# Kernel tuning notes

Hardware: AMD Instinct MI355X
Metric: run time of the kernel (lower is better)

Reference implementation:

```python
import jax, jax.numpy as jnp
import numpy as np

OUTPUT_DIM = 2000
INPUT_DIM = 8192
N_COLS = 2000  # must equal OUTPUT_DIM so bias broadcasts over last dim as in the torch code
SPARSITY = 0.9
BLOCK = 4


def _apply_block_sparsity(weight, block=BLOCK, sparsity=SPARSITY, seed=1234):
    # Zero out 4x4 blocks with probability `sparsity`, mirroring apply_block_sparsity.
    rng = np.random.RandomState(seed)
    rb = (weight.shape[0] + block - 1) // block
    cb = (weight.shape[1] + block - 1) // block
    keep = (rng.rand(rb, cb) <= (1.0 - sparsity)).astype(np.float32)
    mask = np.kron(keep, np.ones((block, block), dtype=np.float32))
    return weight * mask[: weight.shape[0], : weight.shape[1]]


def setup_inputs() -> dict:
    key = jax.random.key(0)
    k_w, k_b, k_x = jax.random.split(key, 3)
    weight = np.asarray(jax.random.normal(k_w, (OUTPUT_DIM, INPUT_DIM), dtype=jnp.float32))
    weight = jnp.asarray(_apply_block_sparsity(weight))
    bias = jax.random.normal(k_b, (OUTPUT_DIM,), dtype=jnp.float32)
    x = jax.random.normal(k_x, (INPUT_DIM, N_COLS), dtype=jnp.float32)
    return {"weight": weight, "bias": bias, "x": x}


def reference(weight, bias, x):
    # [OUT, IN] @ [IN, N] -> [OUT, N]; bias [OUT] broadcasts over last dim (N == OUT here),
    # exactly matching torch.matmul(weight, x) + bias.
    return jnp.matmul(weight, x) + bias
```

## Files before the change

kernel.cpp:

```cpp
#include <hip/hip_runtime.h>

#define K_DIM 8192
#define M_REAL 2000
#define N_REAL 2000
#define M_PAD 2048
#define N_PAD 2048

#define BM 256
#define BN 256
#define BK 32
#define SPLITK 4
#define KSLAB (K_DIM / SPLITK)
#define NIT (KSLAB / BK)

#define NB_CONVW 16384
#define NB_CONVX 4096
#define NB_INIT  3907

typedef __bf16 bf16x8 __attribute__((ext_vector_type(8)));
typedef float f32x4 __attribute__((ext_vector_type(4)));
typedef float fvec4 __attribute__((ext_vector_type(4)));

#define RAW_BARRIER()  asm volatile("s_barrier" ::: "memory")
#define WAIT_VM4()     asm volatile("s_waitcnt vmcnt(4)" ::: "memory")
#define WAIT_VM0()     asm volatile("s_waitcnt vmcnt(0)" ::: "memory")

__device__ __forceinline__ unsigned short f2bf(float f) {
    union { float f; unsigned u; } v; v.f = f;
    unsigned r = v.u + 0x7FFFu + ((v.u >> 16) & 1u);
    return (unsigned short)(r >> 16);
}

__device__ __forceinline__ void async16(const void* g, void* l) {
    __builtin_amdgcn_global_load_lds((__attribute__((address_space(1))) void*)(g),
                                     (__attribute__((address_space(3))) void*)(l),
                                     16, 0, 0);
}

__global__ __launch_bounds__(256) void prep_kernel(const float* __restrict__ W,
                                                   const float* __restrict__ X,
                                                   const float* __restrict__ bias,
                                                   unsigned short* __restrict__ Wb,
                                                   unsigned short* __restrict__ XT,
                                                   float* __restrict__ out) {
    __shared__ unsigned short tile[64][68];
    int bid = blockIdx.x;
    if (bid < NB_CONVW) {
        long long t = (long long)bid * 256 + threadIdx.x;
        long long e = t * 4;
        int m = (int)(e >> 13);
        ushort4 o = make_ushort4(0, 0, 0, 0);
        if (m < M_REAL) {
            fvec4 f = __builtin_nontemporal_load((const fvec4*)(W + e));
            o.x = f2bf(f.x); o.y = f2bf(f.y); o.z = f2bf(f.z); o.w = f2bf(f.w);
        }
        *(ushort4*)(Wb + e) = o;
    } else if (bid < NB_CONVW + NB_CONVX) {
        int b2 = bid - NB_CONVW;
        int k0 = (b2 & 127) * 64;
        int n0 = (b2 >> 7) * 64;
        int t = threadIdx.x;
        int c16 = t & 15, r16 = t >> 4;
#pragma unroll
        for (int it = 0; it < 4; ++it) {
            int k = k0 + r16 + it * 16;
            int n = n0 + c16 * 4;
            fvec4 v = {0.f, 0.f, 0.f, 0.f};
            if (n < N_REAL)
                v = __builtin_nontemporal_load((const fvec4*)(X + (long long)k * N_REAL + n));
            ushort4 o;
            o.x = f2bf(v.x); o.y = f2bf(v.y); o.z = f2bf(v.z); o.w = f2bf(v.w);
            *(ushort4*)&tile[r16 + it * 16][c16 * 4] = o;
        }
        __syncthreads();
#pragma unroll
        for (int it = 0; it < 4; ++it) {
            int nn = r16 + it * 16;
            int k4 = c16 * 4;
            ushort4 o;
            o.x = tile[k4 + 0][nn];
            o.y = tile[k4 + 1][nn];
            o.z = tile[k4 + 2][nn];
            o.w = tile[k4 + 3][nn];
            *(ushort4*)(XT + (long long)(n0 + nn) * K_DIM + k0 + k4) = o;
        }
    } else {
        int t = (bid - NB_CONVW - NB_CONVX) * 256 + threadIdx.x;
        if (t < M_REAL * (N_REAL / 4)) {
            int m = t / (N_REAL / 4);
            int n4 = t - m * (N_REAL / 4);
            float4 bv = *(const float4*)(bias + n4 * 4);
            *(float4*)(out + (long long)m * N_REAL + n4 * 4) = bv;
        }
    }
}

__global__ __launch_bounds__(512, 2) void gemm_kernel(const unsigned short* __restrict__ Wb,
                                                      const unsigned short* __restrict__ XT,
                                                      float* __restrict__ out) {
    __shared__ __align__(16) unsigned short As[2][BM * BK];
    __shared__ __align__(16) unsigned short Bs[2][BN * BK];

    int f = blockIdx.x;
    int xcd = f & 7;
    int local = f >> 3;
    int bz = local & 3;
    int bx = (xcd & 3) * 2 + ((local >> 2) & 1);
    int by = (xcd >> 2) * 4 + (local >> 3);

    int t = threadIdx.x;
    int w = t >> 6;
    int l = t & 63;
    int wm = (w >> 2) * 128;
    int wn = (w & 3) * 64;
    int lane16 = l & 15;
    int quad = l >> 4;
    int m0 = by * BM;
    int n0 = bx * BN;
    int ks = bz * KSLAB;

    f32x4 acc[8][4] = {};

    int srow = l >> 2;
    int scol = (l & 3) * 8;
    int rb = w * 32;
    const unsigned short* gA0 = Wb + (long long)(m0 + rb + srow) * K_DIM + ks + scol;
    const unsigned short* gA1 = gA0 + 16LL * K_DIM;
    const unsigned short* gB0 = XT + (long long)(n0 + rb + srow) * K_DIM + ks + scol;
    const unsigned short* gB1 = gB0 + 16LL * K_DIM;

    async16(gA0, &As[0][rb * BK]);
    async16(gA1, &As[0][(rb + 16) * BK]);
    async16(gB0, &Bs[0][rb * BK]);
    async16(gB1, &Bs[0][(rb + 16) * BK]);
    gA0 += BK; gA1 += BK; gB0 += BK; gB1 += BK;

    for (int kt = 0; kt < NIT; ++kt) {
        int cur = kt & 1;
        if (kt + 1 < NIT) {
            int nxt = cur ^ 1;
            async16(gA0, &As[nxt][rb * BK]);
            async16(gA1, &As[nxt][(rb + 16) * BK]);
            async16(gB0, &Bs[nxt][rb * BK]);
            async16(gB1, &Bs[nxt][(rb + 16) * BK]);
            gA0 += BK; gA1 += BK; gB0 += BK; gB1 += BK;
            WAIT_VM4();
        } else {
            WAIT_VM0();
        }
        RAW_BARRIER();

        bf16x8 a[8], b[4];
#pragma unroll
        for (int i = 0; i < 8; ++i)
            a[i] = *(const bf16x8*)&As[cur][(wm + i * 16 + lane16) * BK + quad * 8];
#pragma unroll
        for (int j = 0; j < 4; ++j)
            b[j] = *(const bf16x8*)&Bs[cur][(wn + j * 16 + lane16) * BK + quad * 8];

#pragma unroll
        for (int i = 0; i < 8; ++i)
#pragma unroll
            for (int j = 0; j < 4; ++j)
                acc[i][j] = __builtin_amdgcn_mfma_f32_16x16x32_bf16(a[i], b[j], acc[i][j], 0, 0, 0);

        if (kt + 1 < NIT)
            RAW_BARRIER();
    }

#pragma unroll
    for (int j = 0; j < 4; ++j) {
        int n = n0 + wn + j * 16 + lane16;
        if (n >= N_REAL) continue;
#pragma unroll
        for (int i = 0; i < 8; ++i) {
            int mbase = m0 + wm + i * 16 + quad * 4;
#pragma unroll
            for (int r = 0; r < 4; ++r) {
                int m = mbase + r;
                if (m < M_REAL)
                    atomicAdd(&out[(long long)m * N_REAL + n], acc[i][j][r]);
            }
        }
    }
}

extern "C" void kernel_launch(void* const* d_in, const int* in_sizes, int n_in,
                              void* d_out, int out_size, void* d_ws, size_t ws_size,
                              hipStream_t stream) {
    const float* W    = (const float*)d_in[0];
    const float* bias = (const float*)d_in[1];
    const float* X    = (const float*)d_in[2];
    float* out = (float*)d_out;

    unsigned short* Wb = (unsigned short*)d_ws;
    unsigned short* XT = Wb + (long long)M_PAD * K_DIM;

    prep_kernel<<<NB_CONVW + NB_CONVX + NB_INIT, 256, 0, stream>>>(W, X, bias, Wb, XT, out);

    gemm_kernel<<<(N_PAD / BN) * (M_PAD / BM) * SPLITK, 512, 0, stream>>>(Wb, XT, out);
}
```

Measured before the change: 266.9 us.

## Widen GEMM tile to 256x512 with 1024-thread blocks and split-K of 8

Doubles the N tile to 512 and the block size to 1024 threads (16 waves), and raises split-K from 4 to 8, so the grid stays at 256 blocks. Each block now reuses its A tile across twice as many columns, which cuts global/L2 traffic per FLOP, and the per-wave load count drops to three async copies per stage. In exchange there are twice as many atomic adds to the output, a larger LDS footprint per block (96KB double-buffered) that likely allows only one block per CU, and shorter K loops that expose more prologue and epilogue overhead.

```diff
diff --git a/kernel.cpp b/kernel.cpp
--- a/kernel.cpp
+++ b/kernel.cpp
@@ -7,9 +7,9 @@
 #define N_PAD 2048
 
 #define BM 256
-#define BN 256
+#define BN 512
 #define BK 32
-#define SPLITK 4
+#define SPLITK 8
 #define KSLAB (K_DIM / SPLITK)
 #define NIT (KSLAB / BK)
 
@@ -22,7 +22,7 @@
 typedef float fvec4 __attribute__((ext_vector_type(4)));
 
 #define RAW_BARRIER()  asm volatile("s_barrier" ::: "memory")
-#define WAIT_VM4()     asm volatile("s_waitcnt vmcnt(4)" ::: "memory")
+#define WAIT_VM3()     asm volatile("s_waitcnt vmcnt(3)" ::: "memory")
 #define WAIT_VM0()     asm volatile("s_waitcnt vmcnt(0)" ::: "memory")
 
 __device__ __forceinline__ unsigned short f2bf(float f) {
@@ -95,24 +95,25 @@
     }
 }
 
-__global__ __launch_bounds__(512, 2) void gemm_kernel(const unsigned short* __restrict__ Wb,
-                                                      const unsigned short* __restrict__ XT,
-                                                      float* __restrict__ out) {
+__global__ __launch_bounds__(1024) void gemm_kernel(const unsigned short* __restrict__ Wb,
+                                                    const unsigned short* __restrict__ XT,
+                                                    float* __restrict__ out) {
     __shared__ __align__(16) unsigned short As[2][BM * BK];
     __shared__ __align__(16) unsigned short Bs[2][BN * BK];
 
     int f = blockIdx.x;
     int xcd = f & 7;
     int local = f >> 3;
-    int bz = local & 3;
-    int bx = (xcd & 3) * 2 + ((local >> 2) & 1);
-    int by = (xcd >> 2) * 4 + (local >> 3);
+    int bz = local & 7;
+    int xy = local >> 3;
+    int bx = xcd & 3;
+    int by = (xcd >> 2) * 4 + xy;
 
     int t = threadIdx.x;
     int w = t >> 6;
     int l = t & 63;
-    int wm = (w >> 2) * 128;
-    int wn = (w & 3) * 64;
+    int wm = (w >> 3) * 128;
+    int wn = (w & 7) * 64;
     int lane16 = l & 15;
     int quad = l >> 4;
     int m0 = by * BM;
@@ -123,28 +124,24 @@
 
     int srow = l >> 2;
     int scol = (l & 3) * 8;
-    int rb = w * 32;
-    const unsigned short* gA0 = Wb + (long long)(m0 + rb + srow) * K_DIM + ks + scol;
-    const unsigned short* gA1 = gA0 + 16LL * K_DIM;
-    const unsigned short* gB0 = XT + (long long)(n0 + rb + srow) * K_DIM + ks + scol;
+    const unsigned short* gA0 = Wb + (long long)(m0 + 16 * w + srow) * K_DIM + ks + scol;
+    const unsigned short* gB0 = XT + (long long)(n0 + 32 * w + srow) * K_DIM + ks + scol;
     const unsigned short* gB1 = gB0 + 16LL * K_DIM;
 
-    async16(gA0, &As[0][rb * BK]);
-    async16(gA1, &As[0][(rb + 16) * BK]);
-    async16(gB0, &Bs[0][rb * BK]);
-    async16(gB1, &Bs[0][(rb + 16) * BK]);
-    gA0 += BK; gA1 += BK; gB0 += BK; gB1 += BK;
+    async16(gA0, &As[0][(16 * w) * BK]);
+    async16(gB0, &Bs[0][(32 * w) * BK]);
+    async16(gB1, &Bs[0][(32 * w + 16) * BK]);
+    gA0 += BK; gB0 += BK; gB1 += BK;
 
     for (int kt = 0; kt < NIT; ++kt) {
         int cur = kt & 1;
         if (kt + 1 < NIT) {
             int nxt = cur ^ 1;
-            async16(gA0, &As[nxt][rb * BK]);
-            async16(gA1, &As[nxt][(rb + 16) * BK]);
-            async16(gB0, &Bs[nxt][rb * BK]);
-            async16(gB1, &Bs[nxt][(rb + 16) * BK]);
-            gA0 += BK; gA1 += BK; gB0 += BK; gB1 += BK;
-            WAIT_VM4();
+            async16(gA0, &As[nxt][(16 * w) * BK]);
+            async16(gB0, &Bs[nxt][(32 * w) * BK]);
+            async16(gB1, &Bs[nxt][(32 * w + 16) * BK]);
+            gA0 += BK; gB0 += BK; gB1 += BK;
+            WAIT_VM3();
         } else {
             WAIT_VM0();
         }
@@ -198,5 +195,5 @@
 
     prep_kernel<<<NB_CONVW + NB_CONVX + NB_INIT, 256, 0, stream>>>(W, X, bias, Wb, XT, out);
 
-    gemm_kernel<<<(N_PAD / BN) * (M_PAD / BM) * SPLITK, 512, 0, stream>>>(Wb, XT, out);
+    gemm_kernel<<<(N_PAD / BN) * (M_PAD / BM) * SPLITK, 1024, 0, stream>>>(Wb, XT, out);
 }
```

Result: slower. 590.5 us (+121.2%).
